# Kernel optimization log

Measured on AMD Instinct MI355X. Metric: run time of the kernel, lower is better.

## Reference

```python
import jax, jax.numpy as jnp
import numpy as np

B, CIN, COUT, N, H, W = 8, 64, 64, 16, 32, 32

def cell_centered_grid(h, w):
    # (h, w, h, w, 4) cell-centered coords in [0,1], then mapped to [-1,1]
    dims = (h, w, h, w)
    axes = [(jnp.arange(d, dtype=jnp.float32) + 0.5) / d for d in dims]
    mesh = jnp.meshgrid(*axes, indexing='ij')
    coords = jnp.stack(mesh, axis=-1)
    return 2.0 * coords - 1.0

def setup_inputs() -> dict:
    key = jax.random.key(0)
    ks = jax.random.split(key, 9)
    v = jax.random.normal(ks[0], (B, CIN, H, W), dtype=jnp.float32)
    params = jax.random.normal(ks[1], (N, COUT, CIN), dtype=jnp.float32) / np.sqrt(N * CIN)
    # coeff_mlp: Linear(4,8) -> GELU -> Linear(8,N), torch default init
    w1 = jax.random.uniform(ks[2], (8, 4), jnp.float32, -1/np.sqrt(4), 1/np.sqrt(4))
    b1 = jax.random.uniform(ks[3], (8,), jnp.float32, -1/np.sqrt(4), 1/np.sqrt(4))
    w2 = jax.random.uniform(ks[4], (N, 8), jnp.float32, -1/np.sqrt(8), 1/np.sqrt(8))
    b2 = jax.random.uniform(ks[5], (N,), jnp.float32, -1/np.sqrt(8), 1/np.sqrt(8))
    # 1x1 conv
    cstd = 1/np.sqrt(CIN)
    conv_w = jax.random.uniform(ks[6], (COUT, CIN), jnp.float32, -cstd, cstd)
    conv_b = jax.random.uniform(ks[7], (COUT,), jnp.float32, -cstd, cstd)
    bias = jax.random.uniform(ks[8], (COUT, 1, 1), jnp.float32, -cstd, cstd)
    return {"v": v, "params": params, "w1": w1, "b1": b1, "w2": w2, "b2": b2,
            "conv_w": conv_w, "conv_b": conv_b, "bias": bias}

def reference(v, params, w1, b1, w2, b2, conv_w, conv_b, bias):
    h, w = v.shape[-2], v.shape[-1]
    coords = cell_centered_grid(h, w)                       # (h1,w1,h2,w2,4)
    hid = jax.nn.gelu(coords @ w1.T + b1, approximate=False)
    coeffs = hid @ w2.T + b2                                # (h1,w1,h2,w2,n)
    # contract coeffs with v over input spatial dims first (small intermediate)
    tmp = jnp.einsum('xyhwn,bixy->bnihw', coeffs, v)        # (B,n,i,h2,w2)
    t = jnp.einsum('bnihw,noi->bohw', tmp, params) / (h * w)
    conv = jnp.einsum('bihw,oi->bohw', v, conv_w) + conv_b[None, :, None, None]
    out = t + conv + bias[None]
    return out
```

## Files before the change

kernel.cpp:

```cpp
#include <hip/hip_runtime.h>
#include <hip/hip_bf16.h>
#include <math.h>

#define WSB_VSUM  0u
#define WSB_GTAB  4096u
#define WSB_LTAB  266240u
#define WSB_QM    528384u
#define WSB_RB2   659456u
#define WSB_WPART 675840u

#define COS8_INIT {0.98078528f, 0.83146961f, 0.55557023f, 0.19509032f, \
                  -0.19509032f, -0.55557023f, -0.83146961f, -0.98078528f}

__device__ inline float gelu_exact(float z) {
    return 0.5f * z * (1.0f + erff(z * 0.70710678118f));
}

__device__ inline float cheb_hwid(const float* w1, int c) {
    return fmaxf((fabsf(w1[c * 4 + 2]) + fabsf(w1[c * 4 + 3])) * (31.0f / 32.0f), 1e-2f);
}

__global__ __launch_bounds__(256) void prep_kernel(const float* __restrict__ params,
                                                   const float* __restrict__ w1,
                                                   const float* __restrict__ b1,
                                                   const float* __restrict__ w2,
                                                   const float* __restrict__ b2,
                                                   char* __restrict__ wsb) {
    const float COS8[8] = COS8_INIT;
    float* Gtab = (float*)(wsb + WSB_GTAB);
    float* Ltab = (float*)(wsb + WSB_LTAB);
    float* Qm   = (float*)(wsb + WSB_QM);
    float* Rb2  = (float*)(wsb + WSB_RB2);
    float* Vsum = (float*)(wsb + WSB_VSUM);
    int u = blockIdx.x * 256 + threadIdx.x;
    if (u < 65536) {
        int xy = u >> 6, cr = u & 63, c = cr >> 3, r = cr & 7;
        float cx = 2.0f * (((xy >> 5) + 0.5f) / 32.0f) - 1.0f;
        float cy = 2.0f * (((xy & 31) + 0.5f) / 32.0f) - 1.0f;
        float z = cx * w1[c * 4 + 0] + cy * w1[c * 4 + 1] + b1[c]
                + cheb_hwid(w1, c) * COS8[r];
        Gtab[u] = gelu_exact(z);
    } else if (u < 131072) {
        int u2 = u - 65536;
        int cr = u2 >> 10, hw = u2 & 1023, c = cr >> 3, r = cr & 7;
        float hwid = cheb_hwid(w1, c);
        float ch = 2.0f * (((hw >> 5) + 0.5f) / 32.0f) - 1.0f;
        float cw = 2.0f * (((hw & 31) + 0.5f) / 32.0f) - 1.0f;
        float vv = ch * w1[c * 4 + 2] + cw * w1[c * 4 + 3];
        float tr = hwid * COS8[r];
        float p = 1.0f, d = 1.0f;
        #pragma unroll
        for (int s = 0; s < 8; s++)
            if (s != r) {
                float ts = hwid * COS8[s];
                p *= (vv - ts);
                d *= (tr - ts);
            }
        Ltab[u2] = p / d;
    } else if (u < 163840) {
        int u2 = u - 131072;
        int c = u2 >> 12, oi = u2 & 4095;
        float s = 0.0f;
        #pragma unroll
        for (int n = 0; n < 16; n++)
            s += params[n * 4096 + oi] * w2[n * 8 + c];
        Qm[u2] = s * (1.0f / 1024.0f);
    } else if (u < 167936) {
        int oi = u - 163840;
        float s = 0.0f;
        #pragma unroll
        for (int n = 0; n < 16; n++)
            s += params[n * 4096 + oi] * b2[n];
        Rb2[oi] = s * (1.0f / 1024.0f);
    } else {
        Vsum[u - 167936] = 0.0f;
    }
}

__global__ __launch_bounds__(256) void wgemm_kernel(const float* __restrict__ v,
                                                    char* __restrict__ wsb) {
    const float* Gtab = (const float*)(wsb + WSB_GTAB);
    float* Wpart = (float*)(wsb + WSB_WPART);
    float* Vsum  = (float*)(wsb + WSB_VSUM);
    __shared__ float Vs[16][68];
    __shared__ float Gs[64][64];
    int t = threadIdx.x;
    int bi0 = blockIdx.x * 16, xy0 = blockIdx.y * 64;
    {
        int r = t >> 4, c4 = t & 15;
        *(float4*)&Vs[r][c4 * 4] = *(const float4*)(v + (bi0 + r) * 1024 + xy0 + c4 * 4);
    }
    #pragma unroll
    for (int l = 0; l < 4; l++) {
        int e = t + l * 256;
        int xy = e >> 4, q = e & 15;
        *(float4*)&Gs[xy][q * 4] = *(const float4*)(Gtab + (size_t)(xy0 + xy) * 64 + q * 4);
    }
    __syncthreads();
    int bl = t >> 4, crq = t & 15;
    float4 acc = make_float4(0.f, 0.f, 0.f, 0.f);
    float vs = 0.0f;
    #pragma unroll 8
    for (int xy = 0; xy < 64; xy++) {
        float a = Vs[bl][xy];
        float4 g = *(const float4*)&Gs[xy][crq * 4];
        acc.x += a * g.x; acc.y += a * g.y; acc.z += a * g.z; acc.w += a * g.w;
        vs += a;
    }
    *(float4*)(Wpart + (size_t)blockIdx.y * 32768 + (bi0 + bl) * 64 + crq * 4) = acc;
    if (crq == 0) atomicAdd(&Vsum[bi0 + bl], vs);
}

__global__ __launch_bounds__(256) void final_kernel(const float* __restrict__ v,
                                                    const float* __restrict__ conv_w,
                                                    const float* __restrict__ conv_b,
                                                    const float* __restrict__ bias,
                                                    float* __restrict__ out,
                                                    char* __restrict__ wsb) {
    const float* Ltab  = (const float*)(wsb + WSB_LTAB);
    const float* Qm    = (const float*)(wsb + WSB_QM);
    const float* Rb2   = (const float*)(wsb + WSB_RB2);
    const float* Vsum  = (const float*)(wsb + WSB_VSUM);
    const float* Wpart = (const float*)(wsb + WSB_WPART);
    __shared__ float smem[128 * 36 + 128 * 64];
    __shared__ float Esh[32];
    float* Ct = smem;
    float* Ys = smem + 128 * 36;
    float* Wsum = Ys;
    int t = threadIdx.x;
    int hw0 = blockIdx.x * 64, o0 = blockIdx.y * 32, b = blockIdx.z;

    {
        int e0 = t * 16;
        float4 a0 = {0,0,0,0}, a1 = {0,0,0,0}, a2 = {0,0,0,0}, a3 = {0,0,0,0};
        const float* wp = Wpart + b * 4096 + e0;
        #pragma unroll
        for (int ks = 0; ks < 16; ks++) {
            const float4* p = (const float4*)(wp + (size_t)ks * 32768);
            float4 x0 = p[0], x1 = p[1], x2 = p[2], x3 = p[3];
            a0.x += x0.x; a0.y += x0.y; a0.z += x0.z; a0.w += x0.w;
            a1.x += x1.x; a1.y += x1.y; a1.z += x1.z; a1.w += x1.w;
            a2.x += x2.x; a2.y += x2.y; a2.z += x2.z; a2.w += x2.w;
            a3.x += x3.x; a3.y += x3.y; a3.z += x3.z; a3.w += x3.w;
        }
        *(float4*)&Wsum[e0]      = a0;
        *(float4*)&Wsum[e0 + 4]  = a1;
        *(float4*)&Wsum[e0 + 8]  = a2;
        *(float4*)&Wsum[e0 + 12] = a3;
    }
    #pragma unroll
    for (int l = 0; l < 8; l++) {
        int e = t + l * 256;
        int kk = e >> 5, ol = e & 31;
        Ct[(64 + kk) * 36 + ol] = conv_w[(o0 + ol) * 64 + kk];
    }
    #pragma unroll
    for (int l = 0; l < 4; l++) {
        int f = t + l * 256;
        int k = f >> 4, q = f & 15;
        *(float4*)&Ys[(64 + k) * 64 + q * 4] =
            *(const float4*)(v + (size_t)b * 65536 + k * 1024 + hw0 + q * 4);
    }
    __syncthreads();

    {
        int ol = t >> 3, c = t & 7;
        float a[8] = {};
        const float* qrow = Qm + c * 4096 + (o0 + ol) * 64;
        for (int i = 0; i < 64; i++) {
            float q = qrow[i];
            float4 w0 = *(const float4*)&Wsum[i * 64 + c * 8];
            float4 w1v = *(const float4*)&Wsum[i * 64 + c * 8 + 4];
            a[0] += q * w0.x; a[1] += q * w0.y; a[2] += q * w0.z; a[3] += q * w0.w;
            a[4] += q * w1v.x; a[5] += q * w1v.y; a[6] += q * w1v.z; a[7] += q * w1v.w;
        }
        #pragma unroll
        for (int r = 0; r < 8; r++)
            Ct[(c * 8 + r) * 36 + ol] = a[r];
    }
    if (t < 32) {
        int o = o0 + t;
        float s = conv_b[o] + bias[o];
        const float* rr = Rb2 + o * 64;
        const float* vs = Vsum + b * 64;
        for (int i = 0; i < 64; i++) s += rr[i] * vs[i];
        Esh[t] = s;
    }
    __syncthreads();

    #pragma unroll
    for (int l = 0; l < 4; l++) {
        int f = t + l * 256;
        int k = f >> 4, q = f & 15;
        *(float4*)&Ys[k * 64 + q * 4] =
            *(const float4*)(Ltab + (size_t)k * 1024 + hw0 + q * 4);
    }
    __syncthreads();

    int ty = t >> 5, tx = t & 31;
    float acc[4][2];
    #pragma unroll
    for (int m = 0; m < 4; m++) {
        float e = Esh[ty * 4 + m];
        acc[m][0] = e; acc[m][1] = e;
    }
    #pragma unroll 4
    for (int k = 0; k < 128; k++) {
        float4 cq = *(const float4*)&Ct[k * 36 + ty * 4];
        float2 y = *(const float2*)&Ys[k * 64 + tx * 2];
        acc[0][0] += cq.x * y.x; acc[0][1] += cq.x * y.y;
        acc[1][0] += cq.y * y.x; acc[1][1] += cq.y * y.y;
        acc[2][0] += cq.z * y.x; acc[2][1] += cq.z * y.y;
        acc[3][0] += cq.w * y.x; acc[3][1] += cq.w * y.y;
    }
    #pragma unroll
    for (int m = 0; m < 4; m++) {
        float2 r = make_float2(acc[m][0], acc[m][1]);
        *(float2*)(out + (size_t)b * 65536 + (o0 + ty * 4 + m) * 1024 + hw0 + tx * 2) = r;
    }
}

extern "C" void kernel_launch(void* const* d_in, const int* in_sizes, int n_in,
                              void* d_out, int out_size, void* d_ws, size_t ws_size,
                              hipStream_t stream) {
    const float* v      = (const float*)d_in[0];
    const float* params = (const float*)d_in[1];
    const float* w1     = (const float*)d_in[2];
    const float* b1     = (const float*)d_in[3];
    const float* w2     = (const float*)d_in[4];
    const float* b2     = (const float*)d_in[5];
    const float* conv_w = (const float*)d_in[6];
    const float* conv_b = (const float*)d_in[7];
    const float* bias   = (const float*)d_in[8];
    float* out = (float*)d_out;
    char* wsb  = (char*)d_ws;

    prep_kernel<<<658, 256, 0, stream>>>(params, w1, b1, w2, b2, wsb);
    wgemm_kernel<<<dim3(32, 16), 256, 0, stream>>>(v, wsb);
    final_kernel<<<dim3(16, 2, 8), 256, 0, stream>>>(v, conv_w, conv_b, bias, out, wsb);
}
```

Measured before the change: 94.55 us.

## Fuse prep kernel into wgemm and replace Vsum atomics with partial sums

Removes the separate prep kernel. The GELU table is recomputed directly into shared memory in each wgemm block, and the Ltab/Qm/Rb2 tables are produced by spare threads of the wgemm blocks. The atomic Vsum accumulation becomes per-block partial sums that final_kernel reduces. This saves one launch and the Gtab round trip through global memory, at the cost of redundant GELU evaluation across blocks.

```diff
diff --git a/kernel.cpp b/kernel.cpp
--- a/kernel.cpp
+++ b/kernel.cpp
@@ -2,12 +2,11 @@
 #include <hip/hip_bf16.h>
 #include <math.h>
 
-#define WSB_VSUM  0u
-#define WSB_GTAB  4096u
-#define WSB_LTAB  266240u
-#define WSB_QM    528384u
-#define WSB_RB2   659456u
-#define WSB_WPART 675840u
+#define WSB_LTAB  0u
+#define WSB_QM    262144u
+#define WSB_RB2   393216u
+#define WSB_WPART 409600u
+#define WSB_VSUMP 2506752u
 
 #define COS8_INIT {0.98078528f, 0.83146961f, 0.55557023f, 0.19509032f, \
                   -0.19509032f, -0.55557023f, -0.83146961f, -0.98078528f}
@@ -20,68 +19,19 @@
     return fmaxf((fabsf(w1[c * 4 + 2]) + fabsf(w1[c * 4 + 3])) * (31.0f / 32.0f), 1e-2f);
 }
 
-__global__ __launch_bounds__(256) void prep_kernel(const float* __restrict__ params,
-                                                   const float* __restrict__ w1,
-                                                   const float* __restrict__ b1,
-                                                   const float* __restrict__ w2,
-                                                   const float* __restrict__ b2,
-                                                   char* __restrict__ wsb) {
+__global__ __launch_bounds__(256) void wgemm_kernel(const float* __restrict__ v,
+                                                    const float* __restrict__ params,
+                                                    const float* __restrict__ w1,
+                                                    const float* __restrict__ b1,
+                                                    const float* __restrict__ w2,
+                                                    const float* __restrict__ b2,
+                                                    char* __restrict__ wsb) {
     const float COS8[8] = COS8_INIT;
-    float* Gtab = (float*)(wsb + WSB_GTAB);
-    float* Ltab = (float*)(wsb + WSB_LTAB);
-    float* Qm   = (float*)(wsb + WSB_QM);
-    float* Rb2  = (float*)(wsb + WSB_RB2);
-    float* Vsum = (float*)(wsb + WSB_VSUM);
-    int u = blockIdx.x * 256 + threadIdx.x;
-    if (u < 65536) {
-        int xy = u >> 6, cr = u & 63, c = cr >> 3, r = cr & 7;
-        float cx = 2.0f * (((xy >> 5) + 0.5f) / 32.0f) - 1.0f;
-        float cy = 2.0f * (((xy & 31) + 0.5f) / 32.0f) - 1.0f;
-        float z = cx * w1[c * 4 + 0] + cy * w1[c * 4 + 1] + b1[c]
-                + cheb_hwid(w1, c) * COS8[r];
-        Gtab[u] = gelu_exact(z);
-    } else if (u < 131072) {
-        int u2 = u - 65536;
-        int cr = u2 >> 10, hw = u2 & 1023, c = cr >> 3, r = cr & 7;
-        float hwid = cheb_hwid(w1, c);
-        float ch = 2.0f * (((hw >> 5) + 0.5f) / 32.0f) - 1.0f;
-        float cw = 2.0f * (((hw & 31) + 0.5f) / 32.0f) - 1.0f;
-        float vv = ch * w1[c * 4 + 2] + cw * w1[c * 4 + 3];
-        float tr = hwid * COS8[r];
-        float p = 1.0f, d = 1.0f;
-        #pragma unroll
-        for (int s = 0; s < 8; s++)
-            if (s != r) {
-                float ts = hwid * COS8[s];
-                p *= (vv - ts);
-                d *= (tr - ts);
-            }
-        Ltab[u2] = p / d;
-    } else if (u < 163840) {
-        int u2 = u - 131072;
-        int c = u2 >> 12, oi = u2 & 4095;
-        float s = 0.0f;
-        #pragma unroll
-        for (int n = 0; n < 16; n++)
-            s += params[n * 4096 + oi] * w2[n * 8 + c];
-        Qm[u2] = s * (1.0f / 1024.0f);
-    } else if (u < 167936) {
-        int oi = u - 163840;
-        float s = 0.0f;
-        #pragma unroll
-        for (int n = 0; n < 16; n++)
-            s += params[n * 4096 + oi] * b2[n];
-        Rb2[oi] = s * (1.0f / 1024.0f);
-    } else {
-        Vsum[u - 167936] = 0.0f;
-    }
-}
-
-__global__ __launch_bounds__(256) void wgemm_kernel(const float* __restrict__ v,
-                                                    char* __restrict__ wsb) {
-    const float* Gtab = (const float*)(wsb + WSB_GTAB);
+    float* Ltab  = (float*)(wsb + WSB_LTAB);
+    float* Qm    = (float*)(wsb + WSB_QM);
+    float* Rb2   = (float*)(wsb + WSB_RB2);
     float* Wpart = (float*)(wsb + WSB_WPART);
-    float* Vsum  = (float*)(wsb + WSB_VSUM);
+    float* VsumP = (float*)(wsb + WSB_VSUMP);
     __shared__ float Vs[16][68];
     __shared__ float Gs[64][64];
     int t = threadIdx.x;
@@ -91,10 +41,15 @@
         *(float4*)&Vs[r][c4 * 4] = *(const float4*)(v + (bi0 + r) * 1024 + xy0 + c4 * 4);
     }
     #pragma unroll
-    for (int l = 0; l < 4; l++) {
+    for (int l = 0; l < 16; l++) {
         int e = t + l * 256;
-        int xy = e >> 4, q = e & 15;
-        *(float4*)&Gs[xy][q * 4] = *(const float4*)(Gtab + (size_t)(xy0 + xy) * 64 + q * 4);
+        int xyl = e >> 6, cr = e & 63, c = cr >> 3, r = cr & 7;
+        int xy = xy0 + xyl;
+        float cx = 2.0f * (((xy >> 5) + 0.5f) / 32.0f) - 1.0f;
+        float cy = 2.0f * (((xy & 31) + 0.5f) / 32.0f) - 1.0f;
+        float z = cx * w1[c * 4 + 0] + cy * w1[c * 4 + 1] + b1[c]
+                + cheb_hwid(w1, c) * COS8[r];
+        Gs[xyl][cr] = gelu_exact(z);
     }
     __syncthreads();
     int bl = t >> 4, crq = t & 15;
@@ -108,7 +63,44 @@
         vs += a;
     }
     *(float4*)(Wpart + (size_t)blockIdx.y * 32768 + (bi0 + bl) * 64 + crq * 4) = acc;
-    if (crq == 0) atomicAdd(&Vsum[bi0 + bl], vs);
+    if (crq == 0) VsumP[blockIdx.y * 512 + bi0 + bl] = vs;
+
+    int bid = blockIdx.y * 32 + blockIdx.x;
+    int u = bid * 200 + t;
+    if (t < 200) {
+        if (u < 65536) {
+            int cr = u >> 10, hw = u & 1023, c = cr >> 3, r = cr & 7;
+            float hwid = cheb_hwid(w1, c);
+            float ch = 2.0f * (((hw >> 5) + 0.5f) / 32.0f) - 1.0f;
+            float cw = 2.0f * (((hw & 31) + 0.5f) / 32.0f) - 1.0f;
+            float vv = ch * w1[c * 4 + 2] + cw * w1[c * 4 + 3];
+            float tr = hwid * COS8[r];
+            float p = 1.0f, d = 1.0f;
+            #pragma unroll
+            for (int s = 0; s < 8; s++)
+                if (s != r) {
+                    float ts = hwid * COS8[s];
+                    p *= (vv - ts);
+                    d *= (tr - ts);
+                }
+            Ltab[u] = p / d;
+        } else if (u < 98304) {
+            int u2 = u - 65536;
+            int c = u2 >> 12, oi = u2 & 4095;
+            float s = 0.0f;
+            #pragma unroll
+            for (int n = 0; n < 16; n++)
+                s += params[n * 4096 + oi] * w2[n * 8 + c];
+            Qm[u2] = s * (1.0f / 1024.0f);
+        } else {
+            int oi = u - 98304;
+            float s = 0.0f;
+            #pragma unroll
+            for (int n = 0; n < 16; n++)
+                s += params[n * 4096 + oi] * b2[n];
+            Rb2[oi] = s * (1.0f / 1024.0f);
+        }
+    }
 }
 
 __global__ __launch_bounds__(256) void final_kernel(const float* __restrict__ v,
@@ -120,10 +112,11 @@
     const float* Ltab  = (const float*)(wsb + WSB_LTAB);
     const float* Qm    = (const float*)(wsb + WSB_QM);
     const float* Rb2   = (const float*)(wsb + WSB_RB2);
-    const float* Vsum  = (const float*)(wsb + WSB_VSUM);
     const float* Wpart = (const float*)(wsb + WSB_WPART);
+    const float* VsumP = (const float*)(wsb + WSB_VSUMP);
     __shared__ float smem[128 * 36 + 128 * 64];
     __shared__ float Esh[32];
+    __shared__ float Vsh[64];
     float* Ct = smem;
     float* Ys = smem + 128 * 36;
     float* Wsum = Ys;
@@ -148,6 +141,12 @@
         *(float4*)&Wsum[e0 + 8]  = a2;
         *(float4*)&Wsum[e0 + 12] = a3;
     }
+    if (t < 64) {
+        float s = 0.0f;
+        #pragma unroll
+        for (int ks = 0; ks < 16; ks++) s += VsumP[ks * 512 + b * 64 + t];
+        Vsh[t] = s;
+    }
     #pragma unroll
     for (int l = 0; l < 8; l++) {
         int e = t + l * 256;
@@ -182,8 +181,7 @@
         int o = o0 + t;
         float s = conv_b[o] + bias[o];
         const float* rr = Rb2 + o * 64;
-        const float* vs = Vsum + b * 64;
-        for (int i = 0; i < 64; i++) s += rr[i] * vs[i];
+        for (int i = 0; i < 64; i++) s += rr[i] * Vsh[i];
         Esh[t] = s;
     }
     __syncthreads();
@@ -235,7 +233,6 @@
     float* out = (float*)d_out;
     char* wsb  = (char*)d_ws;
 
-    prep_kernel<<<658, 256, 0, stream>>>(params, w1, b1, w2, b2, wsb);
-    wgemm_kernel<<<dim3(32, 16), 256, 0, stream>>>(v, wsb);
+    wgemm_kernel<<<dim3(32, 16), 256, 0, stream>>>(v, params, w1, b1, w2, b2, wsb);
     final_kernel<<<dim3(16, 2, 8), 256, 0, stream>>>(v, conv_w, conv_b, bias, out, wsb);
 }
```

Result: faster. 92.68 us (-2.0%).
